# Performance work log

Measured on AMD Instinct MI355X. Metric: run time of the kernel, lower is better.

## Reference

```python
import jax, jax.numpy as jnp
import numpy as np

B, S, D = 1, 2048, 2048
E, K, F = 16, 4, 512
EPS = 1e-6


def setup_inputs() -> dict:
    key = jax.random.key(0)
    ks = jax.random.split(key, 5)
    return {
        "hidden_states": jax.random.normal(ks[0], (B, S, D), dtype=jnp.float32),
        "norm_weight": jnp.ones((D,), dtype=jnp.float32),
        "gate_w": jax.random.normal(ks[1], (E, D), dtype=jnp.float32) * 0.02,
        "w_gate": jax.random.normal(ks[2], (E, D, F), dtype=jnp.float32) * 0.02,
        "w_up": jax.random.normal(ks[3], (E, D, F), dtype=jnp.float32) * 0.02,
        "w_down": jax.random.normal(ks[4], (E, F, D), dtype=jnp.float32) * 0.02,
    }


def _rmsnorm(x, w, eps=EPS):
    xf = x.astype(jnp.float32)
    var = jnp.mean(xf * xf, axis=-1, keepdims=True)
    return (xf * jax.lax.rsqrt(var + eps)).astype(x.dtype) * w


def reference(hidden_states, norm_weight, gate_w, w_gate, w_up, w_down):
    residual = hidden_states
    h = _rmsnorm(hidden_states, norm_weight)
    x = h.reshape(-1, D)                                  # [T, D], T = B*S
    T = x.shape[0]

    # Router: softmax over experts (fp32), top-k, renormalize top-k weights.
    logits = x @ gate_w.T                                  # [T, E]
    probs = jax.nn.softmax(logits.astype(jnp.float32), axis=-1)
    top_w, top_i = jax.lax.top_k(probs, K)                 # [T, K]
    top_w = top_w / jnp.sum(top_w, axis=-1, keepdims=True)
    top_w = top_w.astype(x.dtype)

    # Dense combine matrix [T, E]: routing weight if selected, else 0.
    comb = jnp.zeros((T, E), dtype=x.dtype)
    comb = comb.at[jnp.arange(T)[:, None], top_i].add(top_w)

    # Experts: SiLU-gated MLP per expert, combined with routing weights.
    g = jnp.einsum("td,edf->tef", x, w_gate)               # [T, E, F]
    u = jnp.einsum("td,edf->tef", x, w_up)                 # [T, E, F]
    act = jax.nn.silu(g) * u                               # [T, E, F]
    # Weight per-expert contributions then project down.
    y = jnp.einsum("tef,efd,te->td", act, w_down, comb)    # [T, D]

    out = residual + y.reshape(B, S, D)
    return out
```

## Files before the change

kernel.cpp:

```cpp
#include <hip/hip_runtime.h>
#include <cstdint>
#include <cstddef>

#define T_ 2048
#define D_ 2048
#define E_ 16
#define F_ 512

typedef unsigned short u16;
typedef unsigned int u32;
typedef unsigned long long u64;
typedef __attribute__((ext_vector_type(8))) short bf16x8;
typedef __attribute__((ext_vector_type(4))) float f32x4;
typedef __attribute__((ext_vector_type(2))) u32 u32x2;
typedef __attribute__((ext_vector_type(4))) u32 u32x4;
typedef __attribute__((ext_vector_type(8))) u16 u16x8;

__device__ __forceinline__ u16 f2bf(float f){
  union { float f; u32 u; } c; c.f = f;
  return (u16)((c.u + 0x7FFFu + ((c.u >> 16) & 1u)) >> 16);
}

__device__ __forceinline__ void gload16(const void* g, void* l){
  __builtin_amdgcn_global_load_lds((const __attribute__((address_space(1))) void*)g,
                                   (__attribute__((address_space(3))) void*)l,
                                   16, 0, 0);
}

__device__ __forceinline__ u32 pk2(float a, float b){
  u32 r;
  asm("v_cvt_pk_bf16_f32 %0, %1, %2" : "=v"(r) : "v"(a), "v"(b));
  return r;
}

__global__ __launch_bounds__(256) void k_norm_router(
    const float* __restrict__ x, const float* __restrict__ nw, const float* __restrict__ gw,
    u16* __restrict__ h, int* __restrict__ tok_e, float* __restrict__ tok_w)
{
  const int t = blockIdx.x, tid = threadIdx.x;
  const int lane = tid & 63, wid = tid >> 6;
  const int d0 = tid * 8;
  const float4 v0 = *(const float4*)(x + (size_t)t*D_ + d0);
  const float4 v1 = *(const float4*)(x + (size_t)t*D_ + d0 + 4);
  float hv[8] = {v0.x, v0.y, v0.z, v0.w, v1.x, v1.y, v1.z, v1.w};
  float ss = 0.f;
  #pragma unroll
  for (int j = 0; j < 8; ++j) ss += hv[j]*hv[j];
  #pragma unroll
  for (int o = 32; o; o >>= 1) ss += __shfl_xor(ss, o);
  __shared__ float sred[4];
  __shared__ float red16[4][16];
  __shared__ float lf[16];
  if (lane == 0) sred[wid] = ss;
  __syncthreads();
  const float rstd = rsqrtf((sred[0]+sred[1]+sred[2]+sred[3]) * (1.f/(float)D_) + 1e-6f);
  const float4 w0 = *(const float4*)(nw + d0);
  const float4 w1 = *(const float4*)(nw + d0 + 4);
  const float wv[8] = {w0.x,w0.y,w0.z,w0.w,w1.x,w1.y,w1.z,w1.w};
  #pragma unroll
  for (int j = 0; j < 8; ++j) hv[j] = hv[j] * rstd * wv[j];
  u16x8 hb;
  #pragma unroll
  for (int j = 0; j < 8; ++j) hb[j] = f2bf(hv[j]);
  *(u16x8*)(h + (size_t)t*D_ + d0) = hb;

  float lg[16];
  #pragma unroll
  for (int e = 0; e < 16; ++e){
    const float4 g0 = *(const float4*)(gw + e*D_ + d0);
    const float4 g1 = *(const float4*)(gw + e*D_ + d0 + 4);
    lg[e] = hv[0]*g0.x + hv[1]*g0.y + hv[2]*g0.z + hv[3]*g0.w
          + hv[4]*g1.x + hv[5]*g1.y + hv[6]*g1.z + hv[7]*g1.w;
  }
  #pragma unroll
  for (int e = 0; e < 16; ++e){
    #pragma unroll
    for (int o = 32; o; o >>= 1) lg[e] += __shfl_xor(lg[e], o);
  }
  if (lane == 0){
    #pragma unroll
    for (int e = 0; e < 16; ++e) red16[wid][e] = lg[e];
  }
  __syncthreads();
  if (tid < 16) lf[tid] = red16[0][tid] + red16[1][tid] + red16[2][tid] + red16[3][tid];
  __syncthreads();
  if (tid == 0){
    float l[16];
    #pragma unroll
    for (int e = 0; e < 16; ++e) l[e] = lf[e];
    int sel[4]; float sv[4]; u32 used = 0;
    for (int k = 0; k < 4; ++k){
      float b = -3.4e38f; int bi = 0;
      for (int e = 0; e < 16; ++e)
        if (!((used >> e) & 1u) && l[e] > b){ b = l[e]; bi = e; }
      used |= 1u << bi; sel[k] = bi; sv[k] = b;
    }
    float ex[4]; float s = 0.f;
    for (int k = 0; k < 4; ++k){ ex[k] = __expf(sv[k] - sv[0]); s += ex[k]; }
    const float inv = 1.f / s;
    int4 te = {sel[0], sel[1], sel[2], sel[3]};
    float4 tw4 = {ex[0]*inv, ex[1]*inv, ex[2]*inv, ex[3]*inv};
    *(int4*)(tok_e + t*4) = te;
    *(float4*)(tok_w + t*4) = tw4;
  }
}

__global__ __launch_bounds__(256) void k_build_lists(
    const int* __restrict__ tok_e, const float* __restrict__ tok_w,
    int* __restrict__ eidx, float* __restrict__ ew, int* __restrict__ counts)
{
  const int e = blockIdx.x, tid = threadIdx.x;
  const int lane = tid & 63, wid = tid >> 6;
  __shared__ int wtot[4];
  __shared__ int base;
  if (tid == 0) base = 0;
  __syncthreads();
  for (int t0 = 0; t0 < T_; t0 += 256){
    const int t = t0 + tid;
    const int4 te = *(const int4*)(tok_e + t*4);
    const float4 tw = *(const float4*)(tok_w + t*4);
    bool m = false; float wv = 0.f;
    if      (te.x == e){ m = true; wv = tw.x; }
    else if (te.y == e){ m = true; wv = tw.y; }
    else if (te.z == e){ m = true; wv = tw.z; }
    else if (te.w == e){ m = true; wv = tw.w; }
    const u64 mask = __ballot(m);
    const int pre = __popcll(mask & ((1ull << lane) - 1ull));
    if (lane == 0) wtot[wid] = __popcll(mask);
    __syncthreads();
    int wbase = base;
    for (int i = 0; i < wid; ++i) wbase += wtot[i];
    if (m){
      eidx[e*T_ + wbase + pre] = t;
      ew[e*T_ + wbase + pre] = wv;
    }
    __syncthreads();
    if (tid == 0) base += wtot[0] + wtot[1] + wtot[2] + wtot[3];
    __syncthreads();
  }
  if (tid == 0) counts[e] = base;
}

__global__ __launch_bounds__(256) void k_slots(
    const int* __restrict__ counts, const int* __restrict__ eidx,
    const int* __restrict__ tok_e, int* __restrict__ tok_slot)
{
  const int e = blockIdx.x;
  int abase = 0;
  for (int i = 0; i < e; ++i) abase += counts[i];
  const int cnt = counts[e];
  for (int s = threadIdx.x; s < cnt; s += 256){
    const int t = eidx[e*T_ + s];
    const int4 te = *(const int4*)(tok_e + t*4);
    const int kidx = (te.x == e) ? 0 : (te.y == e) ? 1 : (te.z == e) ? 2 : 3;
    tok_slot[t*4 + kidx] = abase + s;
  }
}

#define WLOADG(KB, SRC, S) do {                                                \
    _Pragma("unroll")                                                          \
    for (int j = 0; j < 4; ++j){                                               \
      const float4 t_ = *(const float4*)((SRC) + (size_t)((KB) + ko*4 + j)*(S));\
      wvf[0][j]=t_.x; wvf[1][j]=t_.y; wvf[2][j]=t_.z; wvf[3][j]=t_.w;          \
    }                                                                          \
  } while (0)

#define WSTOREG(WP) do {                                                       \
    _Pragma("unroll")                                                          \
    for (int i = 0; i < 4; ++i){                                               \
      const int r_ = rg4*4 + i;                                                \
      const u32 idx_ = (u32)(r_*32 + ((ko>>1) ^ (r_&3) ^ ((r_>>2)&3))*8 + (ko&1)*4); \
      u32x2 o_ = { pk2(wvf[i][0], wvf[i][1]), pk2(wvf[i][2], wvf[i][3]) };     \
      *(u32x2*)&(WP)[idx_] = o_;                                               \
    }                                                                          \
  } while (0)

#define WLOADD(KB, SRC, S) do {                                                \
    _Pragma("unroll")                                                          \
    for (int j = 0; j < 2; ++j){                                               \
      const float4 t_ = *(const float4*)((SRC) + (size_t)((KB) + ko*2 + j)*(S));\
      wvf[0][j]=t_.x; wvf[1][j]=t_.y; wvf[2][j]=t_.z; wvf[3][j]=t_.w;          \
    }                                                                          \
  } while (0)

#define WSTORED(WP) do {                                                       \
    _Pragma("unroll")                                                          \
    for (int i = 0; i < 4; ++i){                                               \
      const int r_ = rg4*4 + i;                                                \
      const u32 idx_ = (u32)(r_*32 + ((ko>>2) ^ (r_&3) ^ ((r_>>2)&3))*8 + (ko&3)*2); \
      *(u32*)&(WP)[idx_] = pk2(wvf[i][0], wvf[i][1]);                          \
    }                                                                          \
  } while (0)

__global__ __launch_bounds__(256, 2) void k_gateup(
    const u16* __restrict__ h, const float* __restrict__ wg, const float* __restrict__ wu,
    const int* __restrict__ counts, const int* __restrict__ eidx, const float* __restrict__ ew,
    u16* __restrict__ act)
{
  const int bid = blockIdx.x;
  const int tt = bid >> 7;
  const int e  = (bid >> 3) & 15;
  const int ft = bid & 7;

  const int cnt = counts[e];
  const int row0 = tt * 256;
  if (row0 >= cnt) return;
  int abase = 0;
  for (int i = 0; i < e; ++i) abase += counts[i];

  const int tid = threadIdx.x, lane = tid & 63, w = tid >> 6;
  const int f0 = ft * 64;

  __shared__ __align__(16) u16 Xs[3][8192];
  __shared__ __align__(16) u16 Ws[2][4096];

  int* toksS = (int*)&Xs[0][0];
  if (tid < 256){
    const int slot = row0 + tid;
    const int cs = slot < cnt ? slot : (cnt - 1);
    toksS[tid] = eidx[e*T_ + cs];
  }
  __syncthreads();

  const int lr = lane >> 2, lc = lane & 3;
  const int csw = lc ^ (lr & 3) ^ ((lr >> 2) & 3);
  const u16* srcX[4]; u32 dof[4];
  #pragma unroll
  for (int q = 0; q < 4; ++q){
    const int r = w*64 + q*16 + lr;
    srcX[q] = h + (size_t)toksS[r]*D_ + 8*csw;
    dof[q] = (u32)((w*64 + q*16) * 32);
  }
  const int rg4 = tid & 31, ko = tid >> 5;
  const float* wsel = (rg4 < 16) ? wg : wu;
  const float* srcWf = wsel + (size_t)e*D_*F_ + f0 + ((rg4*4) & 63);
  __syncthreads();

  const int p = lane & 15, g4 = lane >> 4;
  u32 aB[4], bB[8];
  #pragma unroll
  for (int m = 0; m < 4; ++m) aB[m] = (u32)((w*64 + m*16 + p) * 32);
  #pragma unroll
  for (int n = 0; n < 8; ++n) bB[n] = (u32)((n*16 + p) * 32);
  const u32 s8 = 8u * (u32)(g4 ^ (p & 3) ^ ((p >> 2) & 3));

  f32x4 acc[4][8] = {};
  float wvf[4][4];

  WLOADG(0, srcWf, F_);
  #pragma unroll
  for (int q = 0; q < 4; ++q) gload16(srcX[q],      (void*)&Xs[0][dof[q]]);
  #pragma unroll
  for (int q = 0; q < 4; ++q) gload16(srcX[q] + 32, (void*)&Xs[1][dof[q]]);
  asm volatile("s_waitcnt vmcnt(8)" ::: "memory");
  __builtin_amdgcn_sched_barrier(0);
  WSTOREG(&Ws[0][0]);
  asm volatile("s_waitcnt vmcnt(4)" ::: "memory");

  const int NSTEP = D_ / 32;
  int xc = 0;
  for (int kt = 0; kt < NSTEP; ++kt){
    asm volatile("s_waitcnt lgkmcnt(0)" ::: "memory");
    __builtin_amdgcn_s_barrier();
    __builtin_amdgcn_sched_barrier(0);
    if (kt + 1 < NSTEP){
      WLOADG((kt + 1) * 32, srcWf, F_);
      __builtin_amdgcn_sched_barrier(0);
    }
    {
      const u16* Xp = &Xs[xc][0];
      const u16* Wp = &Ws[kt & 1][0];
      bf16x8 aF[4], bF[8];
      #pragma unroll
      for (int m = 0; m < 4; ++m) aF[m] = *(const bf16x8*)&Xp[aB[m] + s8];
      #pragma unroll
      for (int n = 0; n < 8; ++n) bF[n] = *(const bf16x8*)&Wp[bB[n] + s8];
      #pragma unroll
      for (int m = 0; m < 4; ++m)
        #pragma unroll
        for (int n = 0; n < 8; ++n)
          acc[m][n] = __builtin_amdgcn_mfma_f32_16x16x32_bf16(aF[m], bF[n], acc[m][n], 0, 0, 0);
    }
    if (kt + 2 < NSTEP){
      const int kb2 = (kt + 2) * 32;
      int nb = xc + 2; if (nb >= 3) nb -= 3;
      #pragma unroll
      for (int q = 0; q < 4; ++q) gload16(srcX[q] + kb2, (void*)&Xs[nb][dof[q]]);
    }
    if (kt + 1 < NSTEP){
      if (kt + 2 < NSTEP) asm volatile("s_waitcnt vmcnt(4)" ::: "memory");
      else                asm volatile("s_waitcnt vmcnt(0)" ::: "memory");
      __builtin_amdgcn_sched_barrier(0);
      WSTOREG(&Ws[(kt + 1) & 1][0]);
    }
    xc = (xc == 2) ? 0 : xc + 1;
  }

  #pragma unroll
  for (int m = 0; m < 4; ++m)
    #pragma unroll
    for (int r = 0; r < 4; ++r){
      const int row  = w*64 + m*16 + g4*4 + r;
      const int slot = row0 + row;
      if (slot < cnt){
        const float tw = ew[e*T_ + slot];
        #pragma unroll
        for (int n = 0; n < 4; ++n){
          const float gv = acc[m][n][r], uv = acc[m][n+4][r];
          const float a = tw * (gv / (1.f + __expf(-gv))) * uv;
          act[(size_t)(abase + slot)*F_ + f0 + n*16 + p] = f2bf(a);
        }
      }
    }
}

__global__ __launch_bounds__(512, 4) void k_down(
    const u16* __restrict__ act, const float* __restrict__ wd,
    const int* __restrict__ counts, u16* __restrict__ ydown)
{
  const int bid = blockIdx.x;
  const int tt = bid >> 8;
  const int e  = (bid >> 4) & 15;
  const int dt = bid & 15;

  const int cnt = counts[e], row0 = tt * 256;
  if (row0 >= cnt) return;
  int abase = 0;
  for (int i = 0; i < e; ++i) abase += counts[i];

  const int tid = threadIdx.x, lane = tid & 63, w = tid >> 6;
  const int d0 = dt * 128;

  __shared__ __align__(16) u16 As[3][8192];
  __shared__ __align__(16) u16 Wd[2][4096];

  const int lr = lane >> 2, lc = lane & 3;
  const int csw = lc ^ (lr & 3) ^ ((lr >> 2) & 3);
  const u16* srcX[2]; u32 dof[2];
  #pragma unroll
  for (int q = 0; q < 2; ++q){
    const int r = w*32 + q*16 + lr;
    const int rs = (row0 + r < cnt) ? (row0 + r) : (cnt - 1);
    srcX[q] = act + (size_t)(abase + rs)*F_ + 8*csw;
    dof[q] = (u32)((w*32 + q*16) * 32);
  }
  const int rg4 = tid & 31, ko = tid >> 5;
  const float* srcWf = wd + (size_t)e*F_*D_ + d0 + rg4*4;

  const int p = lane & 15, g4 = lane >> 4;
  const int tm = w >> 1, dh = w & 1;
  u32 aB[4], bB[4];
  #pragma unroll
  for (int m = 0; m < 4; ++m) aB[m] = (u32)((tm*64 + m*16 + p) * 32);
  #pragma unroll
  for (int n = 0; n < 4; ++n) bB[n] = (u32)((dh*64 + n*16 + p) * 32);
  const u32 s8 = 8u * (u32)(g4 ^ (p & 3) ^ ((p >> 2) & 3));

  f32x4 acc[4][4] = {};
  float wvf[4][2];

  WLOADD(0, srcWf, D_);
  #pragma unroll
  for (int q = 0; q < 2; ++q) gload16(srcX[q],      (void*)&As[0][dof[q]]);
  #pragma unroll
  for (int q = 0; q < 2; ++q) gload16(srcX[q] + 32, (void*)&As[1][dof[q]]);
  asm volatile("s_waitcnt vmcnt(4)" ::: "memory");
  __builtin_amdgcn_sched_barrier(0);
  WSTORED(&Wd[0][0]);
  asm volatile("s_waitcnt vmcnt(2)" ::: "memory");

  const int NSTEP = F_ / 32;
  int xc = 0;
  for (int kt = 0; kt < NSTEP; ++kt){
    asm volatile("s_waitcnt lgkmcnt(0)" ::: "memory");
    __builtin_amdgcn_s_barrier();
    __builtin_amdgcn_sched_barrier(0);
    if (kt + 1 < NSTEP){
      WLOADD((kt + 1) * 32, srcWf, D_);
      __builtin_amdgcn_sched_barrier(0);
    }
    {
      const u16* Ap = &As[xc][0];
      const u16* Wp = &Wd[kt & 1][0];
      bf16x8 aF[4], bF[4];
      #pragma unroll
      for (int m = 0; m < 4; ++m) aF[m] = *(const bf16x8*)&Ap[aB[m] + s8];
      #pragma unroll
      for (int n = 0; n < 4; ++n) bF[n] = *(const bf16x8*)&Wp[bB[n] + s8];
      #pragma unroll
      for (int m = 0; m < 4; ++m)
        #pragma unroll
        for (int n = 0; n < 4; ++n)
          acc[m][n] = __builtin_amdgcn_mfma_f32_16x16x32_bf16(aF[m], bF[n], acc[m][n], 0, 0, 0);
    }
    if (kt + 2 < NSTEP){
      const int kb2 = (kt + 2) * 32;
      int nb = xc + 2; if (nb >= 3) nb -= 3;
      #pragma unroll
      for (int q = 0; q < 2; ++q) gload16(srcX[q] + kb2, (void*)&As[nb][dof[q]]);
    }
    if (kt + 1 < NSTEP){
      if (kt + 2 < NSTEP) asm volatile("s_waitcnt vmcnt(2)" ::: "memory");
      else                asm volatile("s_waitcnt vmcnt(0)" ::: "memory");
      __builtin_amdgcn_sched_barrier(0);
      WSTORED(&Wd[(kt + 1) & 1][0]);
    }
    xc = (xc == 2) ? 0 : xc + 1;
  }

  #pragma unroll
  for (int m = 0; m < 4; ++m){
    #pragma unroll
    for (int r = 0; r < 4; ++r){
      const int row  = tm*64 + m*16 + g4*4 + r;
      const int slot = row0 + row;
      if (slot < cnt){
        u16* yp = ydown + (size_t)(abase + slot)*D_ + d0 + dh*64;
        #pragma unroll
        for (int n = 0; n < 4; ++n)
          yp[n*16 + p] = f2bf(acc[m][n][r]);
      }
    }
  }
}

__global__ __launch_bounds__(256) void k_combine(
    const float* __restrict__ x, const u16* __restrict__ ydown,
    const int* __restrict__ tok_slot, float* __restrict__ out)
{
  const int t = blockIdx.x;
  const int d0 = threadIdx.x * 8;
  const int4 sl = *(const int4*)(tok_slot + t*4);
  const float4 x0 = *(const float4*)(x + (size_t)t*D_ + d0);
  const float4 x1 = *(const float4*)(x + (size_t)t*D_ + d0 + 4);
  float s[8] = {x0.x, x0.y, x0.z, x0.w, x1.x, x1.y, x1.z, x1.w};
  const int sls[4] = {sl.x, sl.y, sl.z, sl.w};
  #pragma unroll
  for (int k = 0; k < 4; ++k){
    const u16x8 v = *(const u16x8*)(ydown + (size_t)sls[k]*D_ + d0);
    #pragma unroll
    for (int j = 0; j < 8; ++j){
      union { u32 u; float f; } c; c.u = (u32)v[j] << 16;
      s[j] += c.f;
    }
  }
  float4 o0 = {s[0], s[1], s[2], s[3]};
  float4 o1 = {s[4], s[5], s[6], s[7]};
  *(float4*)(out + (size_t)t*D_ + d0)     = o0;
  *(float4*)(out + (size_t)t*D_ + d0 + 4) = o1;
}

extern "C" void kernel_launch(void* const* d_in, const int* in_sizes, int n_in,
                              void* d_out, int out_size, void* d_ws, size_t ws_size,
                              hipStream_t stream)
{
  (void)in_sizes; (void)n_in; (void)out_size; (void)ws_size;
  const float* x     = (const float*)d_in[0];
  const float* nw    = (const float*)d_in[1];
  const float* gw    = (const float*)d_in[2];
  const float* wgate = (const float*)d_in[3];
  const float* wup   = (const float*)d_in[4];
  const float* wdown = (const float*)d_in[5];
  float* out = (float*)d_out;

  char* ws = (char*)d_ws;
  u16*   h        = (u16*)(ws);
  u16*   act      = (u16*)(ws + 8388608);
  int*   counts   = (int*)(ws + 16908288);
  int*   eidx     = (int*)(ws + 16908352);
  float* ew       = (float*)(ws + 17039424);
  int*   tok_e    = (int*)(ws + 17170496);
  float* tok_w    = (float*)(ws + 17203264);
  int*   tok_slot = (int*)(ws + 17236032);
  u16*   ydown    = (u16*)(ws + 17268800);

  k_norm_router<<<T_, 256, 0, stream>>>(x, nw, gw, h, tok_e, tok_w);
  k_build_lists<<<E_, 256, 0, stream>>>(tok_e, tok_w, eidx, ew, counts);
  k_slots<<<E_, 256, 0, stream>>>(counts, eidx, tok_e, tok_slot);
  k_gateup<<<1024, 256, 0, stream>>>(h, wgate, wup, counts, eidx, ew, act);
  k_down<<<2048, 512, 0, stream>>>(act, wdown, counts, ydown);
  k_combine<<<T_, 256, 0, stream>>>(x, ydown, tok_slot, out);
}
```

Before: 171.7 us.

## Split gate/up GEMM along K into two halves with separate activation kernel

Splits the gate/up expert GEMM's reduction dimension into two halves, doubling the grid so more blocks can run concurrently. Each half writes bf16 partial gate and up sums to a new scratch buffer. A new k_act kernel sums the partials, applies SiLU gating and the routing weight, and writes act. k_slots now also scatters routing weights into slot order for k_act. This trades extra global traffic, an extra launch and bf16 rounding of the partial sums for better occupancy and load balance in the gate/up kernel.

After: 191.2 us. +11.4%, slower.

```diff
diff --git a/kernel.cpp b/kernel.cpp
--- a/kernel.cpp
+++ b/kernel.cpp
@@ -15,10 +15,16 @@
 typedef __attribute__((ext_vector_type(2))) u32 u32x2;
 typedef __attribute__((ext_vector_type(4))) u32 u32x4;
 typedef __attribute__((ext_vector_type(8))) u16 u16x8;
+typedef __attribute__((ext_vector_type(4))) u16 u16x4;
 
 __device__ __forceinline__ u16 f2bf(float f){
   union { float f; u32 u; } c; c.f = f;
   return (u16)((c.u + 0x7FFFu + ((c.u >> 16) & 1u)) >> 16);
+}
+
+__device__ __forceinline__ float b2f(u16 v){
+  union { u32 u; float f; } c; c.u = (u32)v << 16;
+  return c.f;
 }
 
 __device__ __forceinline__ void gload16(const void* g, void* l){
@@ -143,7 +149,8 @@
 
 __global__ __launch_bounds__(256) void k_slots(
     const int* __restrict__ counts, const int* __restrict__ eidx,
-    const int* __restrict__ tok_e, int* __restrict__ tok_slot)
+    const float* __restrict__ ew, const int* __restrict__ tok_e,
+    int* __restrict__ tok_slot, float* __restrict__ sw)
 {
   const int e = blockIdx.x;
   int abase = 0;
@@ -154,6 +161,7 @@
     const int4 te = *(const int4*)(tok_e + t*4);
     const int kidx = (te.x == e) ? 0 : (te.y == e) ? 1 : (te.z == e) ? 2 : 3;
     tok_slot[t*4 + kidx] = abase + s;
+    sw[abase + s] = ew[e*T_ + s];
   }
 }
 
@@ -194,13 +202,14 @@
 
 __global__ __launch_bounds__(256, 2) void k_gateup(
     const u16* __restrict__ h, const float* __restrict__ wg, const float* __restrict__ wu,
-    const int* __restrict__ counts, const int* __restrict__ eidx, const float* __restrict__ ew,
-    u16* __restrict__ act)
+    const int* __restrict__ counts, const int* __restrict__ eidx,
+    u16* __restrict__ pbuf)
 {
   const int bid = blockIdx.x;
-  const int tt = bid >> 7;
-  const int e  = (bid >> 3) & 15;
-  const int ft = bid & 7;
+  const int tt = bid >> 8;
+  const int e  = (bid >> 4) & 15;
+  const int ft = (bid >> 1) & 7;
+  const int kh = bid & 1;
 
   const int cnt = counts[e];
   const int row0 = tt * 256;
@@ -210,6 +219,7 @@
 
   const int tid = threadIdx.x, lane = tid & 63, w = tid >> 6;
   const int f0 = ft * 64;
+  const int kbase = kh * 1024;
 
   __shared__ __align__(16) u16 Xs[3][8192];
   __shared__ __align__(16) u16 Ws[2][4096];
@@ -228,12 +238,12 @@
   #pragma unroll
   for (int q = 0; q < 4; ++q){
     const int r = w*64 + q*16 + lr;
-    srcX[q] = h + (size_t)toksS[r]*D_ + 8*csw;
+    srcX[q] = h + (size_t)toksS[r]*D_ + kbase + 8*csw;
     dof[q] = (u32)((w*64 + q*16) * 32);
   }
   const int rg4 = tid & 31, ko = tid >> 5;
   const float* wsel = (rg4 < 16) ? wg : wu;
-  const float* srcWf = wsel + (size_t)e*D_*F_ + f0 + ((rg4*4) & 63);
+  const float* srcWf = wsel + (size_t)e*D_*F_ + (size_t)kbase*F_ + f0 + ((rg4*4) & 63);
   __syncthreads();
 
   const int p = lane & 15, g4 = lane >> 4;
@@ -257,7 +267,7 @@
   WSTOREG(&Ws[0][0]);
   asm volatile("s_waitcnt vmcnt(4)" ::: "memory");
 
-  const int NSTEP = D_ / 32;
+  const int NSTEP = 1024 / 32;
   int xc = 0;
   for (int kt = 0; kt < NSTEP; ++kt){
     asm volatile("s_waitcnt lgkmcnt(0)" ::: "memory");
@@ -296,6 +306,7 @@
     xc = (xc == 2) ? 0 : xc + 1;
   }
 
+  u16* pb = pbuf + ((size_t)kh * 8192 + (size_t)abase) * 1024;
   #pragma unroll
   for (int m = 0; m < 4; ++m)
     #pragma unroll
@@ -303,15 +314,38 @@
       const int row  = w*64 + m*16 + g4*4 + r;
       const int slot = row0 + row;
       if (slot < cnt){
-        const float tw = ew[e*T_ + slot];
+        u16* pr = pb + (size_t)slot*1024 + f0;
         #pragma unroll
         for (int n = 0; n < 4; ++n){
-          const float gv = acc[m][n][r], uv = acc[m][n+4][r];
-          const float a = tw * (gv / (1.f + __expf(-gv))) * uv;
-          act[(size_t)(abase + slot)*F_ + f0 + n*16 + p] = f2bf(a);
+          pr[n*16 + p]       = f2bf(acc[m][n][r]);
+          pr[512 + n*16 + p] = f2bf(acc[m][n+4][r]);
         }
       }
     }
+}
+
+__global__ __launch_bounds__(128) void k_act(
+    const u16* __restrict__ pbuf, const float* __restrict__ sw,
+    u16* __restrict__ act)
+{
+  const int gs = blockIdx.x;
+  const int f = threadIdx.x * 4;
+  const float tw = sw[gs];
+  const u16* p0 = pbuf + (size_t)gs*1024;
+  const u16* p1 = p0 + (size_t)8192*1024;
+  const u16x4 g0 = *(const u16x4*)(p0 + f);
+  const u16x4 g1 = *(const u16x4*)(p1 + f);
+  const u16x4 u0 = *(const u16x4*)(p0 + 512 + f);
+  const u16x4 u1 = *(const u16x4*)(p1 + 512 + f);
+  u16x4 o;
+  #pragma unroll
+  for (int j = 0; j < 4; ++j){
+    const float g = b2f(g0[j]) + b2f(g1[j]);
+    const float u = b2f(u0[j]) + b2f(u1[j]);
+    const float a = tw * (g / (1.f + __expf(-g))) * u;
+    o[j] = f2bf(a);
+  }
+  *(u16x4*)(act + (size_t)gs*F_ + f) = o;
 }
 
 __global__ __launch_bounds__(512, 4) void k_down(
@@ -472,12 +506,15 @@
   int*   tok_e    = (int*)(ws + 17170496);
   float* tok_w    = (float*)(ws + 17203264);
   int*   tok_slot = (int*)(ws + 17236032);
-  u16*   ydown    = (u16*)(ws + 17268800);
+  float* sw       = (float*)(ws + 17268800);
+  u16*   ydown    = (u16*)(ws + 17301568);
+  u16*   pbuf     = (u16*)(ws + 50856000);
 
   k_norm_router<<<T_, 256, 0, stream>>>(x, nw, gw, h, tok_e, tok_w);
   k_build_lists<<<E_, 256, 0, stream>>>(tok_e, tok_w, eidx, ew, counts);
-  k_slots<<<E_, 256, 0, stream>>>(counts, eidx, tok_e, tok_slot);
-  k_gateup<<<1024, 256, 0, stream>>>(h, wgate, wup, counts, eidx, ew, act);
+  k_slots<<<E_, 256, 0, stream>>>(counts, eidx, ew, tok_e, tok_slot, sw);
+  k_gateup<<<2048, 256, 0, stream>>>(h, wgate, wup, counts, eidx, pbuf);
+  k_act<<<8192, 128, 0, stream>>>(pbuf, sw, act);
   k_down<<<2048, 512, 0, stream>>>(act, wdown, counts, ydown);
   k_combine<<<T_, 256, 0, stream>>>(x, ydown, tok_slot, out);
 }
```
